# Kernel tuning notes

Hardware: AMD Instinct MI355X
Metric: run time of the kernel (lower is better)

Reference implementation:

```python
import jax, jax.numpy as jnp
import numpy as np

UNITS = 128
FILTERS = 32
KSIZE = 31
B, T, DV, DQ = 64, 1000, 512, 1024


def setup_inputs() -> dict:
    key = jax.random.key(0)
    ks = jax.random.split(key, 12)
    scale = 0.05
    inp = {
        "query": jax.random.normal(ks[0], (B, DQ), jnp.float32),
        "values": jax.random.normal(ks[1], (B, T, DV), jnp.float32),
        "previous_attention_weights": jax.random.uniform(ks[2], (B, T, 1), jnp.float32),
        # learned params
        "Wq": jax.random.normal(ks[3], (DQ, UNITS), jnp.float32) * scale,
        "bq": jnp.zeros((UNITS,), jnp.float32),
        "Wm": jax.random.normal(ks[4], (DV, UNITS), jnp.float32) * scale,
        "bm": jnp.zeros((UNITS,), jnp.float32),
        "Wv": jax.random.normal(ks[5], (UNITS, 1), jnp.float32) * scale,
        "bv": jnp.zeros((1,), jnp.float32),
        "Wconv": jax.random.normal(ks[6], (KSIZE, 1, FILTERS), jnp.float32) * scale,  # [W, Cin, Cout]
        "Wl": jax.random.normal(ks[7], (FILTERS, UNITS), jnp.float32) * scale,
    }
    return inp


def _forward(query, values, prev_w, Wq, bq, Wm, bm, Wv, bv, Wconv, Wl):
    # location features: Conv1D (same padding, no bias) then Dense(tanh, no bias)
    loc = jax.lax.conv_general_dilated(
        prev_w, Wconv, window_strides=(1,), padding="SAME",
        dimension_numbers=("NWC", "WIO", "NWC"))          # [B, T, FILTERS]
    loc = jnp.tanh(loc @ Wl)                                # [B, T, UNITS]
    q = query @ Wq + bq                                     # [B, UNITS]
    m = values @ Wm + bm                                    # [B, T, UNITS]
    score = jnp.tanh(m + q[:, None, :] + loc) @ Wv + bv     # [B, T, 1]
    attention_weights = jax.nn.softmax(score, axis=1)       # softmax over time
    context = jnp.sum(attention_weights * values, axis=1)   # [B, DV]
    return context, attention_weights


def reference(query, values, previous_attention_weights, Wq, bq, Wm, bm, Wv, bv, Wconv, Wl):
    return _forward(query, values, previous_attention_weights,
                    Wq, bq, Wm, bm, Wv, bv, Wconv, Wl)
```

## Files before the change

### kernel.cpp

```cpp
#include <hip/hip_runtime.h>

#define B_  64
#define T_  1000
#define DV_ 512
#define DQ_ 1024
#define U_  128
#define F_  32
#define KS_ 31

typedef __attribute__((ext_vector_type(8))) short short8;
typedef __attribute__((ext_vector_type(4))) float f32x4;

__device__ __forceinline__ unsigned pk2(float a, float b) {
    union { float f; unsigned u; } x, y;
    x.f = a; y.f = b;
    unsigned ra = (x.u + 0x7FFFu + ((x.u >> 16) & 1u)) >> 16;
    unsigned rb = (y.u + 0x7FFFu + ((y.u >> 16) & 1u)) >> 16;
    return (ra & 0xFFFFu) | (rb << 16);
}

__device__ __forceinline__ float fast_tanh(float x) {
    return 1.0f - 2.0f / (__expf(2.0f * x) + 1.0f);
}

__device__ __forceinline__ short8 pk8(float4 f0, float4 f1) {
    int4 q;
    q.x = pk2(f0.x, f0.y); q.y = pk2(f0.z, f0.w);
    q.z = pk2(f1.x, f1.y); q.w = pk2(f1.z, f1.w);
    return *(short8*)&q;
}

__global__ __launch_bounds__(1024) void prep_kernel(
    const float* __restrict__ Wm, const float* __restrict__ Wl,
    const float* __restrict__ query, const float* __restrict__ Wq,
    short* __restrict__ WmX, short* __restrict__ WlX, float* __restrict__ partQ)
{
    __shared__ float sh[1024];
    int blk = blockIdx.x, tid = threadIdx.x;
    if (blk < 9) {
        int g = blk * 1024 + tid;
        if (g < 8192) {
            int kc = g >> 9, e = g & 511;
            int n = e >> 2, q = e & 3;
            int kb = kc * 32 + q * 8;
            int4 p;
            p.x = pk2(Wm[(kb + 0) * U_ + n], Wm[(kb + 1) * U_ + n]);
            p.y = pk2(Wm[(kb + 2) * U_ + n], Wm[(kb + 3) * U_ + n]);
            p.z = pk2(Wm[(kb + 4) * U_ + n], Wm[(kb + 5) * U_ + n]);
            p.w = pk2(Wm[(kb + 6) * U_ + n], Wm[(kb + 7) * U_ + n]);
            ((int4*)WmX)[g] = p;
        } else if (g < 8704) {
            int e = g - 8192;
            int n = e >> 2, q = e & 3;
            int kb = q * 8;
            int4 p;
            p.x = pk2(Wl[(kb + 0) * U_ + n], Wl[(kb + 1) * U_ + n]);
            p.y = pk2(Wl[(kb + 2) * U_ + n], Wl[(kb + 3) * U_ + n]);
            p.z = pk2(Wl[(kb + 4) * U_ + n], Wl[(kb + 5) * U_ + n]);
            p.w = pk2(Wl[(kb + 6) * U_ + n], Wl[(kb + 7) * U_ + n]);
            ((int4*)WlX)[e] = p;
        }
    } else {
        int id = blk - 9;
        int s  = id >> 3;
        int bg = id & 7;
        sh[tid] = query[(size_t)(bg * 8 + (tid >> 7)) * DQ_ + s * 128 + (tid & 127)];
        __syncthreads();
        int u = tid & 127, h = tid >> 7;
        const float* wp = Wq + (size_t)(s * 128) * U_ + u;
        const float* q0 = sh + h * 128;
        float a0 = 0.f;
#pragma unroll 8
        for (int k = 0; k < 128; ++k) a0 += q0[k] * wp[(size_t)k * U_];
        partQ[s * 8192 + (bg * 8 + h) * 128 + u] = a0;
    }
}

__global__ __launch_bounds__(256) void score_kernel(
    const float* __restrict__ values, const float* __restrict__ prev,
    const float* __restrict__ Wc, const float* __restrict__ Wv,
    const float* __restrict__ bv, const short* __restrict__ WmX,
    const short* __restrict__ WlX, const float* __restrict__ partQ,
    const float* __restrict__ bq, const float* __restrict__ bm,
    float* __restrict__ scores, float* __restrict__ ctxU,
    float* __restrict__ lsum)
{
    __shared__ float WcS[KS_ * F_];
    __shared__ short AsL[64 * 32];
    __shared__ float qbS[U_];
    __shared__ float WvS[U_];
    __shared__ float wS[64];
    __shared__ float4 ps[128];

    const int tid = threadIdx.x;
    const int p = blockIdx.x, b = blockIdx.y;
    const int t0 = p * 64;
    const int nr = (T_ - t0 < 64) ? (T_ - t0) : 64;

    for (int i = tid; i < KS_ * F_; i += 256) WcS[i] = Wc[i];
    if (tid < U_) WvS[tid] = Wv[tid];
    if (tid >= 128) {
        int u = tid - 128;
        float s = bq[u] + bm[u];
#pragma unroll
        for (int sl = 0; sl < 8; ++sl) s += partQ[sl * 8192 + b * 128 + u];
        qbS[u] = s;
    }

    const int wv = tid >> 6, lane = tid & 63;
    const int quad = lane >> 4, m15 = lane & 15;
    const int row0 = wv * 16 + m15;
    const int trow = t0 + row0;
    const int tcl = (trow < T_) ? trow : (T_ - 1);
    const float* aP = values + ((size_t)b * T_ + tcl) * DV_ + quad * 8;
    const int4* bW  = (const int4*)WmX + m15 * 4 + quad;
    const int4* blW = (const int4*)WlX + m15 * 4 + quad;

    float4 aq0[2], aq1[2], aq2[2];
    int4 bf[8];
    aq0[0] = *(const float4*)(aP);      aq0[1] = *(const float4*)(aP + 4);
    aq1[0] = *(const float4*)(aP + 32); aq1[1] = *(const float4*)(aP + 36);
#pragma unroll
    for (int c = 0; c < 8; ++c) bf[c] = bW[c * 64];

    __syncthreads();

    {
        int i = tid & 63, fg = tid >> 6;
        int t = t0 + i;
        const float* pv = prev + b * T_;
        float a8[8] = {};
#pragma unroll
        for (int k = 0; k < KS_; ++k) {
            int tt = t + k - 15;
            float pp = ((unsigned)tt < (unsigned)T_) ? pv[tt] : 0.f;
#pragma unroll
            for (int j = 0; j < 8; ++j) a8[j] += pp * WcS[k * F_ + fg * 8 + j];
        }
        int4 pq;
        pq.x = pk2(a8[0], a8[1]); pq.y = pk2(a8[2], a8[3]);
        pq.z = pk2(a8[4], a8[5]); pq.w = pk2(a8[6], a8[7]);
        ((int4*)AsL)[i * 4 + (fg ^ ((i >> 1) & 3))] = pq;
    }
    __syncthreads();

    f32x4 acc[8] = {};
    {
        short8 afl = ((const short8*)AsL)[row0 * 4 + (quad ^ ((row0 >> 1) & 3))];
#pragma unroll
        for (int c = 0; c < 8; ++c) {
            int4 bl = blW[c * 64];
            acc[c] = __builtin_amdgcn_mfma_f32_16x16x32_bf16(afl, *(short8*)&bl, acc[c], 0, 0, 0);
        }
#pragma unroll
        for (int c = 0; c < 8; ++c) {
            int col = c * 16 + m15;
#pragma unroll
            for (int v = 0; v < 4; ++v)
                acc[c][v] = qbS[col] + fast_tanh(acc[c][v]);
        }
    }

#pragma unroll
    for (int kc = 0; kc < 16; ++kc) {
        if (kc + 2 < 16) {
            aq2[0] = *(const float4*)(aP + (kc + 2) * 32);
            aq2[1] = *(const float4*)(aP + (kc + 2) * 32 + 4);
        }
        short8 af = pk8(aq0[0], aq0[1]);
#pragma unroll
        for (int c = 0; c < 8; ++c) {
            acc[c] = __builtin_amdgcn_mfma_f32_16x16x32_bf16(af, *(short8*)&bf[c], acc[c], 0, 0, 0);
            if (kc + 1 < 16) bf[c] = bW[(kc + 1) * 512 + c * 64];
        }
        aq0[0] = aq1[0]; aq0[1] = aq1[1];
        aq1[0] = aq2[0]; aq1[1] = aq2[1];
    }

    float psum[4] = {};
#pragma unroll
    for (int c = 0; c < 8; ++c) {
        int col = c * 16 + m15;
        float wvv = WvS[col];
#pragma unroll
        for (int v = 0; v < 4; ++v)
            psum[v] += fast_tanh(acc[c][v]) * wvv;
    }
#pragma unroll
    for (int off = 1; off < 16; off <<= 1) {
#pragma unroll
        for (int v = 0; v < 4; ++v) psum[v] += __shfl_xor(psum[v], off);
    }
    if (m15 == 0) {
        float bvv = bv[0];
#pragma unroll
        for (int v = 0; v < 4; ++v) {
            int row = wv * 16 + quad * 4 + v;
            int t = t0 + row;
            float s = psum[v] + bvv;
            if (t < T_) {
                scores[b * T_ + t] = s;
                wS[row] = __expf(s);
            } else {
                wS[row] = 0.f;
            }
        }
    }
    __syncthreads();

    if (tid < 64) {
        float x = wS[tid];
#pragma unroll
        for (int off = 1; off < 64; off <<= 1) x += __shfl_xor(x, off);
        if (tid == 0) atomicAdd(lsum + b, x);
    }

    {
        int cl = tid & 127, tp = tid >> 7;
        const float* vp = values + ((size_t)b * T_ + t0) * DV_ + cl * 4;
        float4 a = {0.f, 0.f, 0.f, 0.f};
#pragma unroll 4
        for (int t = tp; t < nr; t += 2) {
            float4 vv = *(const float4*)(vp + (size_t)t * DV_);
            float wt = wS[t];
            a.x += wt * vv.x; a.y += wt * vv.y; a.z += wt * vv.z; a.w += wt * vv.w;
        }
        if (tp == 1) ps[cl] = a;
        __syncthreads();
        if (tp == 0) {
            float4 o = ps[cl];
            o.x += a.x; o.y += a.y; o.z += a.z; o.w += a.w;
            float* cp = ctxU + (size_t)b * DV_ + cl * 4;
            atomicAdd(cp + 0, o.x);
            atomicAdd(cp + 1, o.y);
            atomicAdd(cp + 2, o.z);
            atomicAdd(cp + 3, o.w);
        }
    }
}

__global__ __launch_bounds__(256) void finish_kernel(
    const float* __restrict__ scores, const float* __restrict__ ctxU,
    const float* __restrict__ lsum, float* __restrict__ attw,
    float* __restrict__ ctx)
{
    int b = blockIdx.x, tid = threadIdx.x;
    float inv = 1.0f / lsum[b];
    {
        const float2* cu = (const float2*)(ctxU + (size_t)b * DV_);
        float2* co = (float2*)(ctx + (size_t)b * DV_);
        float2 v = cu[tid];
        v.x *= inv; v.y *= inv;
        co[tid] = v;
    }
    const float* sb = scores + b * T_;
#pragma unroll
    for (int i = 0; i < 4; ++i) {
        int t = tid + i * 256;
        if (t < T_) attw[b * T_ + t] = __expf(sb[t]) * inv;
    }
}

extern "C" void kernel_launch(void* const* d_in, const int* in_sizes, int n_in,
                              void* d_out, int out_size, void* d_ws, size_t ws_size,
                              hipStream_t stream) {
    const float* query  = (const float*)d_in[0];
    const float* values = (const float*)d_in[1];
    const float* prev   = (const float*)d_in[2];
    const float* Wq     = (const float*)d_in[3];
    const float* bq     = (const float*)d_in[4];
    const float* Wm     = (const float*)d_in[5];
    const float* bm     = (const float*)d_in[6];
    const float* Wv     = (const float*)d_in[7];
    const float* bv     = (const float*)d_in[8];
    const float* Wc     = (const float*)d_in[9];
    const float* Wl     = (const float*)d_in[10];

    float* out  = (float*)d_out;
    float* ctx  = out;
    float* attw = out + B_ * DV_;

    char* ws = (char*)d_ws;
    float* partQ  = (float*)(ws);
    float* scores = (float*)(ws + 262144);
    short* WmX    = (short*)(ws + 524288);
    short* WlX    = (short*)(ws + 655360);
    float* ctxU   = (float*)(ws + 663552);
    float* lsum   = (float*)(ws + 794624);

    hipMemsetAsync(ctxU, 0, B_ * DV_ * sizeof(float) + B_ * sizeof(float), stream);
    prep_kernel<<<73, 1024, 0, stream>>>(Wm, Wl, query, Wq, WmX, WlX, partQ);
    score_kernel<<<dim3(16, B_), 256, 0, stream>>>(values, prev, Wc, Wv, bv,
                                                   WmX, WlX, partQ, bq, bm,
                                                   scores, ctxU, lsum);
    finish_kernel<<<B_, 256, 0, stream>>>(scores, ctxU, lsum, attw, ctx);
}
```

Baseline: 266.4 us.

## Fuse softmax finish into score kernel via last-block counter, drop memset

Removes the separate finish kernel by having the last of the 16 time-tile blocks per batch row, detected with an atomic counter, normalize the context and attention weights. The memset of the accumulators is folded into an extra block of the prep kernel, which also clears the counters. This saves two launches and their gaps, at the cost of extra threadfences and a serialized tail on the last block for each batch row.

After: 464.3 us. +74.3%, slower.

```diff
diff --git a/kernel.cpp b/kernel.cpp
--- a/kernel.cpp
+++ b/kernel.cpp
@@ -33,7 +33,8 @@
 __global__ __launch_bounds__(1024) void prep_kernel(
     const float* __restrict__ Wm, const float* __restrict__ Wl,
     const float* __restrict__ query, const float* __restrict__ Wq,
-    short* __restrict__ WmX, short* __restrict__ WlX, float* __restrict__ partQ)
+    short* __restrict__ WmX, short* __restrict__ WlX, float* __restrict__ partQ,
+    float* __restrict__ ctxU, float* __restrict__ lsum, int* __restrict__ done)
 {
     __shared__ float sh[1024];
     int blk = blockIdx.x, tid = threadIdx.x;
@@ -60,6 +61,9 @@
             p.w = pk2(Wl[(kb + 6) * U_ + n], Wl[(kb + 7) * U_ + n]);
             ((int4*)WlX)[e] = p;
         }
+    } else if (blk == 73) {
+        for (int i = tid; i < B_ * DV_; i += 1024) ctxU[i] = 0.f;
+        if (tid < B_) { lsum[tid] = 0.f; done[tid] = 0; }
     } else {
         int id = blk - 9;
         int s  = id >> 3;
@@ -83,7 +87,8 @@
     const short* __restrict__ WlX, const float* __restrict__ partQ,
     const float* __restrict__ bq, const float* __restrict__ bm,
     float* __restrict__ scores, float* __restrict__ ctxU,
-    float* __restrict__ lsum)
+    float* __restrict__ lsum, int* __restrict__ done,
+    float* __restrict__ attw, float* __restrict__ ctx)
 {
     __shared__ float WcS[KS_ * F_];
     __shared__ short AsL[64 * 32];
@@ -91,6 +96,7 @@
     __shared__ float WvS[U_];
     __shared__ float wS[64];
     __shared__ float4 ps[128];
+    __shared__ int isLast;
 
     const int tid = threadIdx.x;
     const int p = blockIdx.x, b = blockIdx.y;
@@ -237,27 +243,29 @@
             atomicAdd(cp + 3, o.w);
         }
     }
-}
-
-__global__ __launch_bounds__(256) void finish_kernel(
-    const float* __restrict__ scores, const float* __restrict__ ctxU,
-    const float* __restrict__ lsum, float* __restrict__ attw,
-    float* __restrict__ ctx)
-{
-    int b = blockIdx.x, tid = threadIdx.x;
-    float inv = 1.0f / lsum[b];
-    {
+
+    __threadfence();
+    if (tid == 0) {
+        int old = atomicAdd(done + b, 1);
+        isLast = (old == 15);
+    }
+    __syncthreads();
+    if (isLast) {
+        __threadfence();
+        float inv = 1.0f / lsum[b];
         const float2* cu = (const float2*)(ctxU + (size_t)b * DV_);
         float2* co = (float2*)(ctx + (size_t)b * DV_);
-        float2 v = cu[tid];
-        v.x *= inv; v.y *= inv;
-        co[tid] = v;
-    }
-    const float* sb = scores + b * T_;
-#pragma unroll
-    for (int i = 0; i < 4; ++i) {
-        int t = tid + i * 256;
-        if (t < T_) attw[b * T_ + t] = __expf(sb[t]) * inv;
+        if (tid < DV_ / 2) {
+            float2 v = cu[tid];
+            v.x *= inv; v.y *= inv;
+            co[tid] = v;
+        }
+        const float* sb = scores + b * T_;
+#pragma unroll
+        for (int i = 0; i < 4; ++i) {
+            int t = tid + i * 256;
+            if (t < T_) attw[b * T_ + t] = __expf(sb[t]) * inv;
+        }
     }
 }
 
@@ -287,11 +295,12 @@
     short* WlX    = (short*)(ws + 655360);
     float* ctxU   = (float*)(ws + 663552);
     float* lsum   = (float*)(ws + 794624);
-
-    hipMemsetAsync(ctxU, 0, B_ * DV_ * sizeof(float) + B_ * sizeof(float), stream);
-    prep_kernel<<<73, 1024, 0, stream>>>(Wm, Wl, query, Wq, WmX, WlX, partQ);
+    int*   done   = (int*)(ws + 794880);
+
+    prep_kernel<<<74, 1024, 0, stream>>>(Wm, Wl, query, Wq, WmX, WlX, partQ,
+                                         ctxU, lsum, done);
     score_kernel<<<dim3(16, B_), 256, 0, stream>>>(values, prev, Wc, Wv, bv,
                                                    WmX, WlX, partQ, bq, bm,
-                                                   scores, ctxU, lsum);
-    finish_kernel<<<B_, 256, 0, stream>>>(scores, ctxU, lsum, attw, ctx);
-}
+                                                   scores, ctxU, lsum, done,
+                                                   attw, ctx);
+}
```
